# Performance work log

Measured on AMD Instinct MI355X. Metric: run time of the kernel, lower is better.

## Reference

```python
import jax, jax.numpy as jnp
import numpy as np
import math

HIDDEN = 3072
N_HEADS = 32
N_KV_HEADS = 32
HEAD_DIM = HIDDEN // N_HEADS  # 96
ROPE_THETA = 10000.0
ORIG_MAX_POS = 4096
MAX_POS = 131072
SHORT_FACTOR = np.ones(HEAD_DIM // 2, dtype=np.float32)  # length 48 rope scaling factors
SCALING_FACTOR = math.sqrt(1.0 + math.log(MAX_POS / ORIG_MAX_POS) / math.log(ORIG_MAX_POS))


def setup_inputs() -> dict:
    key = jax.random.key(0)
    k1, k2, k3 = jax.random.split(key, 3)
    B, L = 2, 2048
    x = jax.random.normal(k1, (B, L, HIDDEN), dtype=jnp.float32)
    op_size = N_HEADS * HEAD_DIM + 2 * (N_KV_HEADS * HEAD_DIM)
    Wqkv = jax.random.normal(k2, (op_size, HIDDEN), dtype=jnp.float32) * (HIDDEN ** -0.5)
    Wo = jax.random.normal(k3, (HIDDEN, HIDDEN), dtype=jnp.float32) * (HIDDEN ** -0.5)
    return {"x": x, "Wqkv": Wqkv, "Wo": Wo}


def _rope_cos_sin(L):
    # SuScaled RoPE; L <= ORIG_MAX_POS so short_factor is used
    ext = jnp.asarray(SHORT_FACTOR)
    inv_freq_shape = jnp.arange(0, HEAD_DIM, 2, dtype=jnp.float32) / HEAD_DIM
    inv_freq = 1.0 / (ext * (ROPE_THETA ** inv_freq_shape))  # [Hd/2]
    pos = jnp.arange(L, dtype=jnp.float32)
    freqs = pos[:, None] * inv_freq[None, :]  # [L, Hd/2]
    emb = jnp.concatenate([freqs, freqs], axis=-1)  # [L, Hd]
    cos = jnp.cos(emb) * SCALING_FACTOR
    sin = jnp.sin(emb) * SCALING_FACTOR
    return cos[None, None, :, :], sin[None, None, :, :]  # [1,1,L,Hd]


def _rotate_half(t):
    mid = t.shape[-1] // 2
    return jnp.concatenate([-t[..., mid:], t[..., :mid]], axis=-1)


def reference(x, Wqkv, Wo):
    B, L, D = x.shape
    qkv = jnp.einsum('bld,od->blo', x, Wqkv)  # [B,L,op_size]
    qpos = N_HEADS * HEAD_DIM
    kpos = qpos + N_KV_HEADS * HEAD_DIM
    q = qkv[..., :qpos].reshape(B, L, N_HEADS, HEAD_DIM).transpose(0, 2, 1, 3)
    k = qkv[..., qpos:kpos].reshape(B, L, N_KV_HEADS, HEAD_DIM).transpose(0, 2, 1, 3)
    v = qkv[..., kpos:].reshape(B, L, N_KV_HEADS, HEAD_DIM).transpose(0, 2, 1, 3)

    cos, sin = _rope_cos_sin(L)
    q = q * cos + _rotate_half(q) * sin
    k = k * cos + _rotate_half(k) * sin

    scale = HEAD_DIM ** -0.5
    scores = jnp.einsum('bhqd,bhkd->bhqk', q * scale, k)  # [B,H,L,L]
    causal = jnp.triu(jnp.full((L, L), -jnp.inf, dtype=scores.dtype), k=1)
    scores = scores + causal[None, None, :, :]
    probs = jax.nn.softmax(scores, axis=-1)
    out = jnp.einsum('bhqk,bhkd->bhqd', probs, v)  # [B,H,L,Hd]
    out = out.transpose(0, 2, 1, 3).reshape(B, L, N_HEADS * HEAD_DIM)
    return jnp.einsum('blo,do->bld', out, Wo)  # o_proj
```

## Files before the change

### kernel.cpp

```cpp
#include <hip/hip_runtime.h>
#include <cstdint>

typedef short s16x8 __attribute__((ext_vector_type(8)));
typedef float f32x4 __attribute__((ext_vector_type(4)));
typedef unsigned short u16;

#define DEV static __device__ __forceinline__

DEV float bf2f(u16 b) {
  union { unsigned u; float f; } v; v.u = ((unsigned)b) << 16; return v.f;
}
DEV u16 f2bf(float f) {
  union { float f; unsigned u; } v; v.f = f;
  unsigned r = 0x7fffu + ((v.u >> 16) & 1u);
  return (u16)((v.u + r) >> 16);
}

typedef __attribute__((address_space(3))) void lds_void_t;
typedef const __attribute__((address_space(1))) void glob_void_t;

DEV void async_copy16(const void* g, void* l) {
  __builtin_amdgcn_global_load_lds(
      (glob_void_t*)(uintptr_t)g,
      (lds_void_t*)(uint32_t)(uintptr_t)l,
      16, 0, 0);
}

__global__ void cvt_f32_bf16(const float* __restrict__ in, u16* __restrict__ out, int n4) {
  int i = blockIdx.x * 256 + threadIdx.x;
  if (i < n4) {
    const float4 v = reinterpret_cast<const float4*>(in)[i];
    ushort4 o;
    o.x = f2bf(v.x); o.y = f2bf(v.y); o.z = f2bf(v.z); o.w = f2bf(v.w);
    reinterpret_cast<ushort4*>(out)[i] = o;
  }
}

template <bool OUT_BF16>
__global__ __launch_bounds__(256, 2)
void gemm_nt(const u16* __restrict__ A, const u16* __restrict__ B,
             void* __restrict__ C, int M, int N, int K) {
  __shared__ u16 As[128 * 32];
  __shared__ u16 Bs[128 * 32];
  const int tid  = threadIdx.x;
  const int lane = tid & 63;
  const int wave = tid >> 6;
  const int wr = wave >> 1, wc = wave & 1;
  const int l15 = lane & 15, quad = lane >> 4;
  const int bm = blockIdx.x, bn = blockIdx.y;

  const int srow   = lane >> 2;
  const int schunk = (lane & 3) ^ ((srow >> 1) & 3);
  const int fsw    = (l15 >> 1) & 3;

  f32x4 acc[4][4];
  const f32x4 zero4 = {0.f, 0.f, 0.f, 0.f};
#pragma unroll
  for (int i = 0; i < 4; ++i)
#pragma unroll
    for (int j = 0; j < 4; ++j) acc[i][j] = zero4;

  const size_t Abase = (size_t)(bm * 128) * K;
  const size_t Bbase = (size_t)(bn * 128) * K;

  for (int kt = 0; kt < K; kt += 32) {
#pragma unroll
    for (int c = 0; c < 2; ++c) {
      const int grp = wave * 2 + c;
      const int row = grp * 16 + srow;
      const u16* gA = A + Abase + (size_t)row * K + kt + schunk * 8;
      const u16* gB = B + Bbase + (size_t)row * K + kt + schunk * 8;
      async_copy16(gA, As + grp * 512 + lane * 8);
      async_copy16(gB, Bs + grp * 512 + lane * 8);
    }
    __syncthreads();

    s16x8 af[4], bf[4];
#pragma unroll
    for (int mi = 0; mi < 4; ++mi) {
      const int row = wr * 64 + mi * 16 + l15;
      af[mi] = *(const s16x8*)(As + row * 32 + (quad ^ fsw) * 8);
    }
#pragma unroll
    for (int ni = 0; ni < 4; ++ni) {
      const int row = wc * 64 + ni * 16 + l15;
      bf[ni] = *(const s16x8*)(Bs + row * 32 + (quad ^ fsw) * 8);
    }
#pragma unroll
    for (int mi = 0; mi < 4; ++mi)
#pragma unroll
      for (int ni = 0; ni < 4; ++ni)
        acc[mi][ni] = __builtin_amdgcn_mfma_f32_16x16x32_bf16(af[mi], bf[ni], acc[mi][ni], 0, 0, 0);
    __syncthreads();
  }

#pragma unroll
  for (int mi = 0; mi < 4; ++mi) {
#pragma unroll
    for (int ni = 0; ni < 4; ++ni) {
      const int gm0 = bm * 128 + wr * 64 + mi * 16 + quad * 4;
      const int gn  = bn * 128 + wc * 64 + ni * 16 + l15;
#pragma unroll
      for (int r = 0; r < 4; ++r) {
        const size_t idx = (size_t)(gm0 + r) * N + gn;
        if (OUT_BF16) ((u16*)C)[idx] = f2bf(acc[mi][ni][r]);
        else          ((float*)C)[idx] = acc[mi][ni][r];
      }
    }
  }
}

__global__ void rope_split(const u16* __restrict__ qkv, u16* __restrict__ Q,
                           u16* __restrict__ Kb, u16* __restrict__ Vt) {
  const int tok = blockIdx.x;
  const int b = tok >> 11, l = tok & 2047;
  const float pos = (float)l;
  const float SF = 1.1902380714238083f;
  const float QSCALE = 0.10206207261596575f;
  const size_t base = (size_t)tok * 9216;
  for (int i = threadIdx.x; i < 768; i += 256) {
    const int g = i * 4;
    const int h = g / 96, d0 = g - h * 96;
    const ushort4 qv4 = *(const ushort4*)(qkv + base + g);
    const ushort4 kv4 = *(const ushort4*)(qkv + base + 3072 + g);
    const ushort4 vv4 = *(const ushort4*)(qkv + base + 6144 + g);
    const int dp0    = (d0 < 48) ? d0 + 48 : d0 - 48;
    const float sgn  = (d0 < 48) ? -1.0f : 1.0f;
    const ushort4 qp4 = *(const ushort4*)(qkv + base + h * 96 + dp0);
    const ushort4 kp4 = *(const ushort4*)(qkv + base + 3072 + h * 96 + dp0);
    const int fi0 = (d0 < 48) ? d0 : d0 - 48;
    const int bh = b * 32 + h;
    ushort4 qo, ko;
    const u16* qvp = (const u16*)&qv4; const u16* kvp = (const u16*)&kv4;
    const u16* qpp = (const u16*)&qp4; const u16* kpp = (const u16*)&kp4;
    const u16* vvp = (const u16*)&vv4;
    u16* qop = (u16*)&qo; u16* kop = (u16*)&ko;
#pragma unroll
    for (int e = 0; e < 4; ++e) {
      const float inv = exp2f(-13.287712379549449f * ((float)(fi0 + e) * (1.0f / 48.0f)));
      const float ang = pos * inv;
      float s, c;
      sincosf(ang, &s, &c);
      c *= SF; s *= SF;
      const float qout = bf2f(qvp[e]) * c + bf2f(qpp[e]) * sgn * s;
      const float kout = bf2f(kvp[e]) * c + bf2f(kpp[e]) * sgn * s;
      qop[e] = f2bf(qout * QSCALE);
      kop[e] = f2bf(kout);
      Vt[((size_t)bh * 96 + d0 + e) * 2048 + l] = vvp[e];
    }
    *(ushort4*)(Q  + ((size_t)bh * 2048 + l) * 96 + d0) = qo;
    *(ushort4*)(Kb + ((size_t)bh * 2048 + l) * 96 + d0) = ko;
  }
}

__global__ __launch_bounds__(256, 2)
void attn(const u16* __restrict__ Q, const u16* __restrict__ Kb,
          const u16* __restrict__ Vt, u16* __restrict__ ctx) {
  const int qb = 31 - blockIdx.x;
  const int bh = blockIdx.y;
  const int tid = threadIdx.x, lane = tid & 63, wave = tid >> 6;
  const int l15 = lane & 15, quad = lane >> 4;

  __shared__ alignas(16) u16 Kl[2][64 * 104];
  __shared__ alignas(16) u16 Vl[2][96 * 64];
  __shared__ alignas(16) u16 Pl[4][16][80];

  const size_t hbase = (size_t)bh * 2048 * 96;
  const int q0 = qb * 64 + wave * 16;

  s16x8 aq[3];
#pragma unroll
  for (int c = 0; c < 3; ++c)
    aq[c] = *(const s16x8*)(Q + hbase + (size_t)(q0 + l15) * 96 + c * 32 + quad * 8);

  float m_[4] = {-1e30f, -1e30f, -1e30f, -1e30f};
  float l_[4] = {0.f, 0.f, 0.f, 0.f};
  f32x4 o[6];
  const f32x4 zero4 = {0.f, 0.f, 0.f, 0.f};
#pragma unroll
  for (int d = 0; d < 6; ++d) o[d] = zero4;

  auto stage = [&](int buf, int kb) {
    const int k0 = kb * 64;
    for (int j = wave; j < 13; j += 4) {
      const int id = j * 64 + lane;
      const int k  = id / 13;
      const int cc = id - k * 13;
      const u16* src = Kb + hbase + (size_t)(k0 + k) * 96 + (cc < 12 ? cc * 8 : 0);
      async_copy16(src, &Kl[buf][j * 512 + lane * 8]);
    }
    for (int j = wave; j < 12; j += 4) {
      const int id = j * 64 + lane;
      const int d  = id >> 3;
      const int lc = (id & 7) ^ (d & 7);
      const u16* src = Vt + ((size_t)bh * 96 + d) * 2048 + k0 + lc * 8;
      async_copy16(src, &Vl[buf][j * 512 + lane * 8]);
    }
  };

  stage(0, 0);
  __syncthreads();
  int cur = 0;

  for (int kb = 0; kb <= qb; ++kb) {
    if (kb < qb) stage(cur ^ 1, kb + 1);
    const int k0 = kb * 64;
    const bool last = (kb == qb);
    const int nsub   = last ? (wave + 1) : 4;
    const int nchunk = last ? ((wave >> 1) + 1) : 2;
    const int nsw    = nchunk * 2;

    f32x4 s[4];
#pragma unroll
    for (int sub = 0; sub < 4; ++sub) {
      if (sub < nsub) {
        const u16* kr = &Kl[cur][(sub * 16 + l15) * 104 + quad * 8];
        const s16x8 b0 = *(const s16x8*)(kr);
        const s16x8 b1 = *(const s16x8*)(kr + 32);
        const s16x8 b2 = *(const s16x8*)(kr + 64);
        f32x4 t = __builtin_amdgcn_mfma_f32_16x16x32_bf16(aq[0], b0, zero4, 0, 0, 0);
        t = __builtin_amdgcn_mfma_f32_16x16x32_bf16(aq[1], b1, t, 0, 0, 0);
        t = __builtin_amdgcn_mfma_f32_16x16x32_bf16(aq[2], b2, t, 0, 0, 0);
        s[sub] = t;
      } else {
        s[sub] = (f32x4){-1e30f, -1e30f, -1e30f, -1e30f};
      }
    }

    if (last) {
#pragma unroll
      for (int sub = 0; sub < 4; ++sub)
#pragma unroll
        for (int r = 0; r < 4; ++r) {
          const int row = q0 + quad * 4 + r;
          const int col = k0 + sub * 16 + l15;
          if (col > row) s[sub][r] = -1e30f;
        }
    }

    float alpha[4];
#pragma unroll
    for (int r = 0; r < 4; ++r) {
      float mx = fmaxf(fmaxf(s[0][r], s[1][r]), fmaxf(s[2][r], s[3][r]));
#pragma unroll
      for (int off = 8; off >= 1; off >>= 1) mx = fmaxf(mx, __shfl_xor(mx, off));
      const float mn = fmaxf(m_[r], mx);
      alpha[r] = __expf(m_[r] - mn);
      const float p0 = __expf(s[0][r] - mn);
      const float p1 = __expf(s[1][r] - mn);
      const float p2 = __expf(s[2][r] - mn);
      const float p3 = __expf(s[3][r] - mn);
      s[0][r] = p0; s[1][r] = p1; s[2][r] = p2; s[3][r] = p3;
      float rs = (p0 + p1) + (p2 + p3);
#pragma unroll
      for (int off = 8; off >= 1; off >>= 1) rs += __shfl_xor(rs, off);
      l_[r] = l_[r] * alpha[r] + rs;
      m_[r] = mn;
    }
#pragma unroll
    for (int d = 0; d < 6; ++d)
#pragma unroll
      for (int r = 0; r < 4; ++r) o[d][r] *= alpha[r];

#pragma unroll
    for (int sub = 0; sub < 4; ++sub) {
      if (sub < nsw) {
#pragma unroll
        for (int r = 0; r < 4; ++r)
          Pl[wave][quad * 4 + r][sub * 16 + l15] = f2bf(s[sub][r]);
      }
    }

#pragma unroll
    for (int c = 0; c < 2; ++c) {
      if (c < nchunk) {
        const s16x8 ap = *(const s16x8*)(&Pl[wave][l15][c * 32 + quad * 8]);
#pragma unroll
        for (int dblk = 0; dblk < 6; ++dblk) {
          const int d = dblk * 16 + l15;
          const s16x8 bv = *(const s16x8*)(&Vl[cur][d * 64 + (((c * 4 + quad) ^ (d & 7)) * 8)]);
          o[dblk] = __builtin_amdgcn_mfma_f32_16x16x32_bf16(ap, bv, o[dblk], 0, 0, 0);
        }
      }
    }

    __syncthreads();
    cur ^= 1;
  }

  const int b = bh >> 5, h = bh & 31;
  float invl[4];
#pragma unroll
  for (int r = 0; r < 4; ++r) invl[r] = 1.0f / l_[r];
#pragma unroll
  for (int d = 0; d < 6; ++d)
#pragma unroll
    for (int r = 0; r < 4; ++r) {
      const int row = q0 + quad * 4 + r;
      ctx[((size_t)(b * 2048 + row)) * 3072 + h * 96 + d * 16 + l15] = f2bf(o[d][r] * invl[r]);
    }
}

extern "C" void kernel_launch(void* const* d_in, const int* in_sizes, int n_in,
                              void* d_out, int out_size, void* d_ws, size_t ws_size,
                              hipStream_t stream) {
  const float* x    = (const float*)d_in[0];
  const float* Wqkv = (const float*)d_in[1];
  const float* Wo   = (const float*)d_in[2];
  float* out = (float*)d_out;

  char* ws = (char*)d_ws;
  u16* wq_b  = (u16*)(ws);
  u16* wo_b  = (u16*)(ws + 56623104);
  u16* x_b   = (u16*)(ws + 75497472);
  u16* qkv_b = (u16*)(ws + 100663296);
  u16* K_b   = (u16*)(ws + 176160768);
  u16* Vt_b  = (u16*)(ws + 201326592);
  u16* Q_b   = x_b;
  u16* ctx_b = qkv_b;

  cvt_f32_bf16<<<27648, 256, 0, stream>>>(Wqkv, wq_b, 28311552 / 4);
  cvt_f32_bf16<<<9216,  256, 0, stream>>>(Wo,   wo_b,  9437184 / 4);
  cvt_f32_bf16<<<12288, 256, 0, stream>>>(x,    x_b,  12582912 / 4);

  gemm_nt<true><<<dim3(32, 72), 256, 0, stream>>>(x_b, wq_b, (void*)qkv_b, 4096, 9216, 3072);

  rope_split<<<4096, 256, 0, stream>>>(qkv_b, Q_b, K_b, Vt_b);

  attn<<<dim3(32, 64), 256, 0, stream>>>(Q_b, K_b, Vt_b, ctx_b);

  gemm_nt<false><<<dim3(32, 24), 256, 0, stream>>>(ctx_b, wo_b, (void*)out, 4096, 3072, 3072);
}
```

Baseline: 1.006 ms.

## Compute transposed S tile and pass P through registers via bpermute, dropping LDS

```diff
diff --git a/kernel.cpp b/kernel.cpp
--- a/kernel.cpp
+++ b/kernel.cpp
@@ -153,7 +153,7 @@
   }
 }
 
-__global__ __launch_bounds__(256, 2)
+__global__ __launch_bounds__(256, 3)
 void attn(const u16* __restrict__ Q, const u16* __restrict__ Kb,
           const u16* __restrict__ Vt, u16* __restrict__ ctx) {
   const int qb = 31 - blockIdx.x;
@@ -163,7 +163,6 @@
 
   __shared__ alignas(16) u16 Kl[2][64 * 104];
   __shared__ alignas(16) u16 Vl[2][96 * 64];
-  __shared__ alignas(16) u16 Pl[4][16][80];
 
   const size_t hbase = (size_t)bh * 2048 * 96;
   const int q0 = qb * 64 + wave * 16;
@@ -173,8 +172,7 @@
   for (int c = 0; c < 3; ++c)
     aq[c] = *(const s16x8*)(Q + hbase + (size_t)(q0 + l15) * 96 + c * 32 + quad * 8);
 
-  float m_[4] = {-1e30f, -1e30f, -1e30f, -1e30f};
-  float l_[4] = {0.f, 0.f, 0.f, 0.f};
+  float m_ = -1e30f, l_ = 0.f;
   f32x4 o[6];
   const f32x4 zero4 = {0.f, 0.f, 0.f, 0.f};
 #pragma unroll
@@ -202,13 +200,16 @@
   __syncthreads();
   int cur = 0;
 
+  const int addrA = (l15 + (quad & 1) * 32) * 4;
+  const int addrB = addrA + 64;
+  const bool hb = (quad >= 2);
+
   for (int kb = 0; kb <= qb; ++kb) {
     if (kb < qb) stage(cur ^ 1, kb + 1);
     const int k0 = kb * 64;
     const bool last = (kb == qb);
     const int nsub   = last ? (wave + 1) : 4;
     const int nchunk = last ? ((wave >> 1) + 1) : 2;
-    const int nsw    = nchunk * 2;
 
     f32x4 s[4];
 #pragma unroll
@@ -218,9 +219,9 @@
         const s16x8 b0 = *(const s16x8*)(kr);
         const s16x8 b1 = *(const s16x8*)(kr + 32);
         const s16x8 b2 = *(const s16x8*)(kr + 64);
-        f32x4 t = __builtin_amdgcn_mfma_f32_16x16x32_bf16(aq[0], b0, zero4, 0, 0, 0);
-        t = __builtin_amdgcn_mfma_f32_16x16x32_bf16(aq[1], b1, t, 0, 0, 0);
-        t = __builtin_amdgcn_mfma_f32_16x16x32_bf16(aq[2], b2, t, 0, 0, 0);
+        f32x4 t = __builtin_amdgcn_mfma_f32_16x16x32_bf16(b0, aq[0], zero4, 0, 0, 0);
+        t = __builtin_amdgcn_mfma_f32_16x16x32_bf16(b1, aq[1], t, 0, 0, 0);
+        t = __builtin_amdgcn_mfma_f32_16x16x32_bf16(b2, aq[2], t, 0, 0, 0);
         s[sub] = t;
       } else {
         s[sub] = (f32x4){-1e30f, -1e30f, -1e30f, -1e30f};
@@ -228,58 +229,76 @@
     }
 
     if (last) {
+      const int q = q0 + l15;
 #pragma unroll
       for (int sub = 0; sub < 4; ++sub)
 #pragma unroll
         for (int r = 0; r < 4; ++r) {
-          const int row = q0 + quad * 4 + r;
-          const int col = k0 + sub * 16 + l15;
-          if (col > row) s[sub][r] = -1e30f;
+          const int k = k0 + sub * 16 + quad * 4 + r;
+          if (k > q) s[sub][r] = -1e30f;
         }
     }
 
-    float alpha[4];
-#pragma unroll
-    for (int r = 0; r < 4; ++r) {
-      float mx = fmaxf(fmaxf(s[0][r], s[1][r]), fmaxf(s[2][r], s[3][r]));
-#pragma unroll
-      for (int off = 8; off >= 1; off >>= 1) mx = fmaxf(mx, __shfl_xor(mx, off));
-      const float mn = fmaxf(m_[r], mx);
-      alpha[r] = __expf(m_[r] - mn);
-      const float p0 = __expf(s[0][r] - mn);
-      const float p1 = __expf(s[1][r] - mn);
-      const float p2 = __expf(s[2][r] - mn);
-      const float p3 = __expf(s[3][r] - mn);
-      s[0][r] = p0; s[1][r] = p1; s[2][r] = p2; s[3][r] = p3;
-      float rs = (p0 + p1) + (p2 + p3);
-#pragma unroll
-      for (int off = 8; off >= 1; off >>= 1) rs += __shfl_xor(rs, off);
-      l_[r] = l_[r] * alpha[r] + rs;
-      m_[r] = mn;
-    }
+    float mx = s[0][0];
+#pragma unroll
+    for (int sub = 0; sub < 4; ++sub)
+#pragma unroll
+      for (int r = 0; r < 4; ++r) mx = fmaxf(mx, s[sub][r]);
+    mx = fmaxf(mx, __shfl_xor(mx, 16));
+    mx = fmaxf(mx, __shfl_xor(mx, 32));
+    const float mn = fmaxf(m_, mx);
+    const float al = __expf(m_ - mn);
+    m_ = mn;
+#pragma unroll
+    for (int sub = 0; sub < 4; ++sub)
+#pragma unroll
+      for (int r = 0; r < 4; ++r) s[sub][r] = __expf(s[sub][r] - mn);
+    float rs = (((s[0][0] + s[0][1]) + (s[0][2] + s[0][3])) +
+                ((s[1][0] + s[1][1]) + (s[1][2] + s[1][3]))) +
+               (((s[2][0] + s[2][1]) + (s[2][2] + s[2][3])) +
+                ((s[3][0] + s[3][1]) + (s[3][2] + s[3][3])));
+    rs += __shfl_xor(rs, 16);
+    rs += __shfl_xor(rs, 32);
+    l_ = l_ * al + rs;
+
+    float alr[4];
+#pragma unroll
+    for (int r = 0; r < 4; ++r)
+      alr[r] = __int_as_float(__builtin_amdgcn_ds_bpermute((quad * 4 + r) * 4,
+                                                           __float_as_int(al)));
 #pragma unroll
     for (int d = 0; d < 6; ++d)
 #pragma unroll
-      for (int r = 0; r < 4; ++r) o[d][r] *= alpha[r];
-
+      for (int r = 0; r < 4; ++r) o[d][r] *= alr[r];
+
+    unsigned pk[4][2];
 #pragma unroll
     for (int sub = 0; sub < 4; ++sub) {
-      if (sub < nsw) {
-#pragma unroll
-        for (int r = 0; r < 4; ++r)
-          Pl[wave][quad * 4 + r][sub * 16 + l15] = f2bf(s[sub][r]);
-      }
+      asm("v_cvt_pk_bf16_f32 %0, %1, %2" : "=v"(pk[sub][0]) : "v"(s[sub][0]), "v"(s[sub][1]));
+      asm("v_cvt_pk_bf16_f32 %0, %1, %2" : "=v"(pk[sub][1]) : "v"(s[sub][2]), "v"(s[sub][3]));
     }
 
 #pragma unroll
     for (int c = 0; c < 2; ++c) {
       if (c < nchunk) {
-        const s16x8 ap = *(const s16x8*)(&Pl[wave][l15][c * 32 + quad * 8]);
+        const int a00 = __builtin_amdgcn_ds_bpermute(addrA, (int)pk[c * 2][0]);
+        const int a01 = __builtin_amdgcn_ds_bpermute(addrA, (int)pk[c * 2][1]);
+        const int a10 = __builtin_amdgcn_ds_bpermute(addrA, (int)pk[c * 2 + 1][0]);
+        const int a11 = __builtin_amdgcn_ds_bpermute(addrA, (int)pk[c * 2 + 1][1]);
+        const int b00 = __builtin_amdgcn_ds_bpermute(addrB, (int)pk[c * 2][0]);
+        const int b01 = __builtin_amdgcn_ds_bpermute(addrB, (int)pk[c * 2][1]);
+        const int b10 = __builtin_amdgcn_ds_bpermute(addrB, (int)pk[c * 2 + 1][0]);
+        const int b11 = __builtin_amdgcn_ds_bpermute(addrB, (int)pk[c * 2 + 1][1]);
+        union { s16x8 v; int u[4]; } ap;
+        ap.u[0] = hb ? a10 : a00;
+        ap.u[1] = hb ? a11 : a01;
+        ap.u[2] = hb ? b10 : b00;
+        ap.u[3] = hb ? b11 : b01;
 #pragma unroll
         for (int dblk = 0; dblk < 6; ++dblk) {
           const int d = dblk * 16 + l15;
           const s16x8 bv = *(const s16x8*)(&Vl[cur][d * 64 + (((c * 4 + quad) ^ (d & 7)) * 8)]);
-          o[dblk] = __builtin_amdgcn_mfma_f32_16x16x32_bf16(ap, bv, o[dblk], 0, 0, 0);
+          o[dblk] = __builtin_amdgcn_mfma_f32_16x16x32_bf16(ap.v, bv, o[dblk], 0, 0, 0);
         }
       }
     }
@@ -291,7 +310,10 @@
   const int b = bh >> 5, h = bh & 31;
   float invl[4];
 #pragma unroll
-  for (int r = 0; r < 4; ++r) invl[r] = 1.0f / l_[r];
+  for (int r = 0; r < 4; ++r) {
+    const int v = __builtin_amdgcn_ds_bpermute((quad * 4 + r) * 4, __float_as_int(l_));
+    invl[r] = 1.0f / __int_as_float(v);
+  }
 #pragma unroll
   for (int d = 0; d < 6; ++d)
 #pragma unroll
```

Measured after the change: 908.0 us. 1.11x faster.
